# Kernel tuning notes

Measured on AMD Instinct MI355X. Metric: run time of the kernel, lower is better.

The kernel has to match this reference:

```python
import jax, jax.numpy as jnp
import numpy as np

NEIGH_W = 0.25  # self.neigh_w
act = jax.nn.leaky_relu  # negative_slope=0.01, matches nn.LeakyReLU default


def _lin(x, w, b):
    # torch Linear with weight stored as [in, out]
    return x @ w + b


def setup_inputs() -> dict:
    key = jax.random.key(0)
    I, C, L = 1024, 32, 64  # images, curves/image, points/curve (uniform segments)
    N = I * C * L
    ks = jax.random.split(key, 32)

    def p(k, shape, scale=0.1):
        return jax.random.normal(k, shape, dtype=jnp.float32) * scale

    curve_tensor = jax.random.normal(ks[0], (N, 8), dtype=jnp.float32)
    # segment-boundary labels: col1 = curve start (every L rows), col0 = image start (every L*C rows)
    lab = np.zeros((N, 2), np.int64)
    lab[::L, 1] = 1
    lab[::L * C, 0] = 1
    curve_label = jnp.asarray(lab)
    cors_batch = jax.random.normal(ks[1], (I, C, C, 5), dtype=jnp.float32)

    inp = dict(curve_tensor=curve_tensor, curve_label=curve_label, cors_batch=cors_batch)
    dims = [("crv_mlp", 8, 8), ("crv_lv1", 24, 32), ("crv_lv2", 32, 24),
            ("inter1", 24, 24), ("inter2", 24, 24),
            ("grp1", 72, 24), ("grp2", 24, 24), ("grp3", 24, 24),
            ("img1", 24, 18), ("img2", 18, 12), ("img3", 12, 6)]
    for i, (name, din, dout) in enumerate(dims):
        inp[name + "_w"] = p(ks[2 + 2 * i], (din, dout))
        inp[name + "_b"] = p(ks[3 + 2 * i], (dout,))
    # cor_mlp is initialized to all ones (cor_init_rand=0 in the original)
    inp["cor_w"] = jnp.ones((5, 24), jnp.float32)
    inp["cor_b"] = jnp.ones((24,), jnp.float32)
    return inp


def reference(curve_tensor, curve_label, cors_batch,
              crv_mlp_w, crv_mlp_b, crv_lv1_w, crv_lv1_b, crv_lv2_w, crv_lv2_b,
              inter1_w, inter1_b, inter2_w, inter2_b, cor_w, cor_b,
              grp1_w, grp1_b, grp2_w, grp2_b, grp3_w, grp3_b,
              img1_w, img1_b, img2_w, img2_b, img3_w, img3_b):
    I, C = cors_batch.shape[0], cors_batch.shape[1]
    L = curve_tensor.shape[0] // (I * C)

    # ---- curve level: ring-graph roll aggregation within each curve segment ----
    x = curve_tensor.reshape(I * C, L, 8)

    def agg(t):
        neigh = _lin(jnp.roll(t, 1, axis=1), crv_mlp_w, crv_mlp_b) \
              + _lin(jnp.roll(t, -1, axis=1), crv_mlp_w, crv_mlp_b)
        return NEIGH_W * neigh + (1.0 - 2.0 * NEIGH_W) * t

    x1 = agg(x)
    x2 = agg(x1)
    embed = jnp.concatenate([x, x1, x2], axis=-1)            # [I*C, L, 24]
    feat = act(_lin(act(_lin(embed, crv_lv1_w, crv_lv1_b)), crv_lv2_w, crv_lv2_b))
    group = feat.mean(axis=1)                                 # [I*C, 24] per-curve feature
    group = act(_lin(act(_lin(group, inter1_w, inter1_b)), inter2_w, inter2_b))

    # ---- image level: pairwise cor-weighted aggregation over curves per image ----
    g = group.reshape(I, C, 24)
    cor = act(_lin(cors_batch, cor_w, cor_b))                 # [I, C, C, 24]

    def cagg(t):
        # after[i,j,d] = sum_k before[i,k,d] * cor[i,j,k,d]
        return jnp.einsum('ikd,ijkd->ijd', t, cor)

    g1 = cagg(g)
    g2 = cagg(g1)
    emb = jnp.concatenate([g, g1, g2], axis=-1)               # [I, C, 72]
    h = act(_lin(act(_lin(act(_lin(emb, grp1_w, grp1_b)), grp2_w, grp2_b)), grp3_w, grp3_b))
    img = h.mean(axis=1)                                      # [I, 24]

    out = _lin(act(_lin(act(_lin(img, img1_w, img1_b)), img2_w, img2_b)), img3_w, img3_b)
    return jax.nn.sigmoid(out)                                # [I, brands]
```

## Files before the change

### kernel.cpp

```cpp
#include <hip/hip_runtime.h>
#include <hip/hip_bf16.h>
#include <math.h>

#define LEAKY(x) fmaxf((x), 0.01f * (x))

typedef float v2f __attribute__((ext_vector_type(2)));
typedef __bf16 bf8 __attribute__((ext_vector_type(8)));
typedef float f4 __attribute__((ext_vector_type(4)));

constexpr int IMGS = 1024;
constexpr int CRV  = 32;
constexpr int LPT  = 64;

__device__ __forceinline__ void ldseg(float* dst, const float* __restrict__ src,
                                      int n, int tid, int nt) {
  for (int i = tid; i < n; i += nt) dst[i] = src[i];
}

__device__ __forceinline__ f4 leaky4(f4 x) {
  return __builtin_elementwise_max(x, x * 0.01f);
}

__device__ __forceinline__ float ring_sum(float v) {
  int s = __builtin_bit_cast(int, v);
  int a = __builtin_amdgcn_update_dpp(0, s, 0x134, 0xF, 0xF, false);
  int b = __builtin_amdgcn_update_dpp(0, s, 0x13C, 0xF, 0xF, false);
  return __builtin_bit_cast(float, a) + __builtin_bit_cast(float, b);
}

__device__ __forceinline__ float row_sum16(float v) {
  int s;
  s = __builtin_amdgcn_update_dpp(0, __builtin_bit_cast(int, v), 0x121, 0xF, 0xF, false);
  v += __builtin_bit_cast(float, s);
  s = __builtin_amdgcn_update_dpp(0, __builtin_bit_cast(int, v), 0x122, 0xF, 0xF, false);
  v += __builtin_bit_cast(float, s);
  s = __builtin_amdgcn_update_dpp(0, __builtin_bit_cast(int, v), 0x124, 0xF, 0xF, false);
  v += __builtin_bit_cast(float, s);
  s = __builtin_amdgcn_update_dpp(0, __builtin_bit_cast(int, v), 0x128, 0xF, 0xF, false);
  v += __builtin_bit_cast(float, s);
  return v;
}

__device__ __forceinline__ unsigned bfpair(float x, float y) {
  __hip_bfloat162 h = __float22bfloat162_rn(make_float2(x, y));
  unsigned r;
  __builtin_memcpy(&r, &h, 4);
  return r;
}

__device__ __forceinline__ unsigned bfr(float x) {
  unsigned u = __builtin_bit_cast(unsigned, x);
  return u + 0x7fffu + ((u >> 16) & 1u);
}
__device__ __forceinline__ unsigned bfpair_fast(float x, float y) {
  return __builtin_amdgcn_perm(bfr(y), bfr(x), 0x07060302u);
}

#define WOFF(pp, cc) (((pp) << 4) + ((((cc) + ((pp) >> 1)) & 3) << 2))

__device__ float w1eff_val(const float* mw, const float* mb,
                           const float* w1, const float* b1, int n, int k) {
  if (k < 8) {
    return w1[k * 32 + n] + 0.5f * w1[(8 + k) * 32 + n] + 0.25f * w1[(16 + k) * 32 + n];
  } else if (k < 16) {
    int a = k - 8;
    float s = 0.f;
    for (int i = 0; i < 8; i++)
      s += mw[a * 8 + i] * (w1[(8 + i) * 32 + n] + w1[(16 + i) * 32 + n]);
    return 0.25f * s;
  } else if (k < 24) {
    int a = k - 16;
    float s = 0.f;
    for (int i = 0; i < 8; i++) {
      float m2 = 0.f;
      for (int c = 0; c < 8; c++) m2 += mw[a * 8 + c] * mw[c * 8 + i];
      s += m2 * w1[(16 + i) * 32 + n];
    }
    return 0.0625f * s;
  } else if (k == 24) {
    float s = b1[n];
    for (int i = 0; i < 8; i++) {
      s += mb[i] * (0.5f * w1[(8 + i) * 32 + n] + 0.75f * w1[(16 + i) * 32 + n]);
      float wb = 0.f;
      for (int c = 0; c < 8; c++) wb += mb[c] * mw[c * 8 + i];
      s += 0.25f * wb * w1[(16 + i) * 32 + n];
    }
    return s;
  }
  return 0.f;
}

__global__ __launch_bounds__(256) void prep_kernel(
    const float* __restrict__ mw, const float* __restrict__ mb,
    const float* __restrict__ w1, const float* __restrict__ b1,
    const float* __restrict__ w2, const float* __restrict__ b2,
    const float* __restrict__ i1w, const float* __restrict__ i2w,
    unsigned* __restrict__ fragA1, unsigned* __restrict__ fragA2,
    float* __restrict__ fragC,
    float* __restrict__ i1wT, float* __restrict__ i2wT)
{
  const int tid = threadIdx.x;
  for (int idx = tid; idx < 512; idx += 256) {
    int tile = idx >> 8;
    int lane = (idx >> 2) & 63;
    int word = idx & 3;
    int n  = tile * 16 + (lane & 15);
    int k0 = (lane >> 4) * 8 + word * 2;
    fragA1[idx] = bfpair(w1eff_val(mw, mb, w1, b1, n, k0),
                         w1eff_val(mw, mb, w1, b1, n, k0 + 1));
    float u0 = (n < 24) ? w2[k0 * 24 + n] : 0.f;
    float u1 = (n < 24) ? w2[(k0 + 1) * 24 + n] : 0.f;
    fragA2[idx] = bfpair(u0, u1);
  }
  for (int idx = tid; idx < 512; idx += 256) {
    int tile = idx >> 8;
    int lane = (idx >> 2) & 63;
    int r = idx & 3;
    int n = tile * 16 + ((lane >> 4) & 3) * 4 + r;
    fragC[idx] = (n < 24) ? b2[n] : 0.f;
  }
  for (int idx = tid; idx < 576; idx += 256) {
    int jj = idx / 24, ii = idx - jj * 24;
    i1wT[idx] = i1w[ii * 24 + jj];
    i2wT[idx] = i2w[ii * 24 + jj];
  }
}

__global__ __launch_bounds__(256) void curve_kernel(
    const float* __restrict__ ct,
    const unsigned* __restrict__ fragA1, const unsigned* __restrict__ fragA2,
    const float* __restrict__ fragC,
    const float* __restrict__ i1wT, const float* __restrict__ i1b,
    const float* __restrict__ i2wT, const float* __restrict__ i2b,
    float* __restrict__ gout)
{
  __shared__ __align__(16) unsigned sX[4][2][1024];
  __shared__ __align__(16) float    srow[4][2][32];

  const int tid  = threadIdx.x;
  const int wave = tid >> 6;
  const int lane = tid & 63;
  const int curve0 = blockIdx.x * 8 + wave * 2;

  uint4 awv[2], a2v[2];
  float4 cbv[2];
  #pragma unroll
  for (int mt = 0; mt < 2; mt++) {
    awv[mt] = *(const uint4*)(fragA1 + mt * 256 + lane * 4);
    a2v[mt] = *(const uint4*)(fragA2 + mt * 256 + lane * 4);
    cbv[mt] = *(const float4*)(fragC + mt * 256 + lane * 4);
  }

  const float* pA = ct + ((size_t)curve0 * LPT + lane) * 8;
  const float* pB = pA + LPT * 8;
  float4 a0 = *(const float4*)pA;
  float4 a1 = *(const float4*)(pA + 4);
  float4 b0 = *(const float4*)pB;
  float4 b1v = *(const float4*)(pB + 4);

  float xA[8], xB[8];
  xA[0] = a0.x; xA[1] = a0.y; xA[2] = a0.z; xA[3] = a0.w;
  xA[4] = a1.x; xA[5] = a1.y; xA[6] = a1.z; xA[7] = a1.w;
  xB[0] = b0.x; xB[1] = b0.y; xB[2] = b0.z; xB[3] = b0.w;
  xB[4] = b1v.x; xB[5] = b1v.y; xB[6] = b1v.z; xB[7] = b1v.w;

  float s1A[8], t2A[8], s1B[8], t2B[8];
  #pragma unroll
  for (int i = 0; i < 8; i++) s1A[i] = ring_sum(xA[i]);
  #pragma unroll
  for (int i = 0; i < 8; i++) s1B[i] = ring_sum(xB[i]);
  #pragma unroll
  for (int i = 0; i < 8; i++) t2A[i] = ring_sum(s1A[i]);
  #pragma unroll
  for (int i = 0; i < 8; i++) t2B[i] = ring_sum(s1B[i]);

  unsigned* Xw0 = &sX[wave][0][0];
  unsigned* Xw1 = &sX[wave][1][0];
  {
    uint4 wv;
    wv.x = bfpair_fast(xA[0], xA[1]);  wv.y = bfpair_fast(xA[2], xA[3]);
    wv.z = bfpair_fast(xA[4], xA[5]);  wv.w = bfpair_fast(xA[6], xA[7]);
    *(uint4*)&Xw0[WOFF(lane, 0)] = wv;
    wv.x = bfpair_fast(s1A[0], s1A[1]); wv.y = bfpair_fast(s1A[2], s1A[3]);
    wv.z = bfpair_fast(s1A[4], s1A[5]); wv.w = bfpair_fast(s1A[6], s1A[7]);
    *(uint4*)&Xw0[WOFF(lane, 1)] = wv;
    wv.x = bfpair_fast(t2A[0], t2A[1]); wv.y = bfpair_fast(t2A[2], t2A[3]);
    wv.z = bfpair_fast(t2A[4], t2A[5]); wv.w = bfpair_fast(t2A[6], t2A[7]);
    *(uint4*)&Xw0[WOFF(lane, 2)] = wv;
    wv.x = 0x00003f80u; wv.y = 0u; wv.z = 0u; wv.w = 0u;
    *(uint4*)&Xw0[WOFF(lane, 3)] = wv;

    wv.x = bfpair_fast(xB[0], xB[1]);  wv.y = bfpair_fast(xB[2], xB[3]);
    wv.z = bfpair_fast(xB[4], xB[5]);  wv.w = bfpair_fast(xB[6], xB[7]);
    *(uint4*)&Xw1[WOFF(lane, 0)] = wv;
    wv.x = bfpair_fast(s1B[0], s1B[1]); wv.y = bfpair_fast(s1B[2], s1B[3]);
    wv.z = bfpair_fast(s1B[4], s1B[5]); wv.w = bfpair_fast(s1B[6], s1B[7]);
    *(uint4*)&Xw1[WOFF(lane, 1)] = wv;
    wv.x = bfpair_fast(t2B[0], t2B[1]); wv.y = bfpair_fast(t2B[2], t2B[3]);
    wv.z = bfpair_fast(t2B[4], t2B[5]); wv.w = bfpair_fast(t2B[6], t2B[7]);
    *(uint4*)&Xw1[WOFF(lane, 2)] = wv;
    wv.x = 0x00003f80u; wv.y = 0u; wv.z = 0u; wv.w = 0u;
    *(uint4*)&Xw1[WOFF(lane, 3)] = wv;
  }
  __builtin_amdgcn_wave_barrier();

  const int q   = lane >> 4;
  const int c16 = lane & 15;

  #pragma unroll
  for (int cv = 0; cv < 2; cv++) {
    unsigned* Xw = cv ? Xw1 : Xw0;
    f4 d[2][4];
    bf8 bx[4];
    #pragma unroll
    for (int nt = 0; nt < 4; nt++)
      bx[nt] = __builtin_bit_cast(bf8, *(const uint4*)&Xw[WOFF(c16 + nt * 16, q)]);
    const f4 z = (f4){0.f, 0.f, 0.f, 0.f};
    #pragma unroll
    for (int mt = 0; mt < 2; mt++) {
      bf8 aw = __builtin_bit_cast(bf8, awv[mt]);
      #pragma unroll
      for (int nt = 0; nt < 4; nt++)
        d[mt][nt] = __builtin_amdgcn_mfma_f32_16x16x32_bf16(aw, bx[nt], z, 0, 0, 0);
    }
    #pragma unroll
    for (int mt = 0; mt < 2; mt++) {
      #pragma unroll
      for (int nt = 0; nt < 4; nt++) {
        f4 v = leaky4(d[mt][nt]);
        const int prow = nt * 16 + c16;
        const int word = WOFF(prow, mt * 2 + (q >> 1)) + (q & 1) * 2;
        uint2 pk; pk.x = bfpair_fast(v.x, v.y); pk.y = bfpair_fast(v.z, v.w);
        *(uint2*)&Xw[word] = pk;
      }
    }
  }
  __builtin_amdgcn_wave_barrier();

  #pragma unroll
  for (int cv = 0; cv < 2; cv++) {
    unsigned* Xw = cv ? Xw1 : Xw0;
    f4 d2[2][4];
    bf8 bh[4];
    #pragma unroll
    for (int nt = 0; nt < 4; nt++)
      bh[nt] = __builtin_bit_cast(bf8, *(const uint4*)&Xw[WOFF(c16 + nt * 16, q)]);
    #pragma unroll
    for (int mt = 0; mt < 2; mt++) {
      bf8 a2 = __builtin_bit_cast(bf8, a2v[mt]);
      f4 cb_ = __builtin_bit_cast(f4, cbv[mt]);
      #pragma unroll
      for (int nt = 0; nt < 4; nt++)
        d2[mt][nt] = __builtin_amdgcn_mfma_f32_16x16x32_bf16(a2, bh[nt], cb_, 0, 0, 0);
    }
    float m8[2][4];
    #pragma unroll
    for (int mt = 0; mt < 2; mt++) {
      f4 t = leaky4(d2[mt][0]) + leaky4(d2[mt][1]);
      t = t + leaky4(d2[mt][2]);
      t = t + leaky4(d2[mt][3]);
      #pragma unroll
      for (int r = 0; r < 4; r++)
        m8[mt][r] = row_sum16(t[r]) * (1.0f / 64.0f);
    }
    if (c16 == 0) {
      f4 v0 = (f4){m8[0][0], m8[0][1], m8[0][2], m8[0][3]};
      *(f4*)&srow[wave][cv][q * 4] = v0;
      if (q < 2) {
        f4 v1 = (f4){m8[1][0], m8[1][1], m8[1][2], m8[1][3]};
        *(f4*)&srow[wave][cv][16 + q * 4] = v1;
      }
    }
  }
  __builtin_amdgcn_wave_barrier();

  const int half = lane >> 5;
  const int l32  = lane & 31;
  const int jd   = (l32 < 24) ? l32 : 0;
  float* srw = &srow[wave][half][0];

  float sv[24];
  #pragma unroll
  for (int i = 0; i < 24; i++) sv[i] = srw[i];

  float a = i1b[jd];
  #pragma unroll
  for (int t = 0; t < 6; t++) {
    float4 wv = *(const float4*)&i1wT[jd * 24 + t * 4];
    a += sv[t * 4 + 0] * wv.x + sv[t * 4 + 1] * wv.y
       + sv[t * 4 + 2] * wv.z + sv[t * 4 + 3] * wv.w;
  }
  a = LEAKY(a);
  if (l32 < 24) srw[l32] = a;
  __builtin_amdgcn_wave_barrier();

  float av[24];
  #pragma unroll
  for (int i = 0; i < 24; i++) av[i] = srw[i];

  float o = i2b[jd];
  #pragma unroll
  for (int t = 0; t < 6; t++) {
    float4 wv = *(const float4*)&i2wT[jd * 24 + t * 4];
    o += av[t * 4 + 0] * wv.x + av[t * 4 + 1] * wv.y
       + av[t * 4 + 2] * wv.z + av[t * 4 + 3] * wv.w;
  }
  o = LEAKY(o);

  if (l32 < 24) gout[(size_t)(curve0 + half) * 24 + l32] = o;
}

__global__ __launch_bounds__(768) void image_kernel(
    const float* __restrict__ cors, const float* __restrict__ gin,
    const float* __restrict__ cw,  const float* __restrict__ cb,
    const float* __restrict__ g1w, const float* __restrict__ g1b,
    const float* __restrict__ g2w, const float* __restrict__ g2b,
    const float* __restrict__ g3w, const float* __restrict__ g3b,
    const float* __restrict__ m1w, const float* __restrict__ m1b,
    const float* __restrict__ m2w, const float* __restrict__ m2b,
    const float* __restrict__ m3w, const float* __restrict__ m3b,
    float* __restrict__ out)
{
  __shared__ __align__(16) float sCorsP[CRV * CRV * 8];
  __shared__ __align__(16) float sG0[CRV * 24], sG1[CRV * 24], sG2[CRV * 24];
  __shared__ __align__(16) float sHa[CRV * 24], sHb[CRV * 24];
  __shared__ float sW1[1728], sW2[576], sW3[576];
  __shared__ float sT[96];

  const int tid = threadIdx.x;
  const int img = blockIdx.x;
  const int j = tid / 24;
  const int d = tid - j * 24;

  {
    const float* cbase = cors + (size_t)img * (CRV * CRV * 5);
    for (int idx = tid; idx < CRV * CRV * 5; idx += 768) {
      int jj = idx / 160;
      int r  = idx - jj * 160;
      int k  = r / 5;
      int c  = r - k * 5;
      sCorsP[(jj * CRV + k) * 8 + c] = cbase[idx];
    }
  }
  sG0[tid] = gin[(size_t)img * (CRV * 24) + tid];
  ldseg(sW1, g1w, 1728, tid, 768);
  ldseg(sW2, g2w, 576, tid, 768);
  ldseg(sW3, g3w, 576, tid, 768);
  float wc0 = cw[0 * 24 + d], wc1 = cw[1 * 24 + d], wc2 = cw[2 * 24 + d];
  float wc3 = cw[3 * 24 + d], wc4 = cw[4 * 24 + d];
  float cbd = cb[d];
  float g1bd = g1b[d], g2bd = g2b[d], g3bd = g3b[d];
  __syncthreads();

  float corv[CRV];
  #pragma unroll
  for (int k = 0; k < CRV; k++) {
    const float* cr = &sCorsP[(j * CRV + k) * 8];
    float4 qq = *(const float4*)cr;
    float q4 = cr[4];
    float v = cbd + qq.x * wc0 + qq.y * wc1 + qq.z * wc2 + qq.w * wc3 + q4 * wc4;
    corv[k] = LEAKY(v);
  }
  {
    float t1 = 0.0f;
    #pragma unroll
    for (int k = 0; k < CRV; k++) t1 += sG0[k * 24 + d] * corv[k];
    sG1[j * 24 + d] = t1;
  }
  __syncthreads();
  {
    float t2 = 0.0f;
    #pragma unroll
    for (int k = 0; k < CRV; k++) t2 += sG1[k * 24 + d] * corv[k];
    sG2[j * 24 + d] = t2;
  }
  __syncthreads();
  {
    float v = g1bd;
    #pragma unroll
    for (int i = 0; i < 24; i++) v += sG0[j * 24 + i] * sW1[i * 24 + d];
    #pragma unroll
    for (int i = 0; i < 24; i++) v += sG1[j * 24 + i] * sW1[(24 + i) * 24 + d];
    #pragma unroll
    for (int i = 0; i < 24; i++) v += sG2[j * 24 + i] * sW1[(48 + i) * 24 + d];
    sHa[j * 24 + d] = LEAKY(v);
  }
  __syncthreads();
  {
    float v = g2bd;
    #pragma unroll
    for (int i = 0; i < 24; i++) v += sHa[j * 24 + i] * sW2[i * 24 + d];
    sHb[j * 24 + d] = LEAKY(v);
  }
  __syncthreads();
  {
    float v = g3bd;
    #pragma unroll
    for (int i = 0; i < 24; i++) v += sHb[j * 24 + i] * sW3[i * 24 + d];
    sHa[j * 24 + d] = LEAKY(v);
  }
  __syncthreads();
  if (tid < 24) {
    float s = 0.0f;
    #pragma unroll
    for (int k = 0; k < CRV; k++) s += sHa[k * 24 + tid];
    sT[tid] = s * (1.0f / CRV);
  }
  __syncthreads();
  if (tid < 18) {
    float v = m1b[tid];
    #pragma unroll
    for (int i = 0; i < 24; i++) v += sT[i] * m1w[i * 18 + tid];
    sT[32 + tid] = LEAKY(v);
  }
  __syncthreads();
  if (tid < 12) {
    float v = m2b[tid];
    #pragma unroll
    for (int i = 0; i < 18; i++) v += sT[32 + i] * m2w[i * 12 + tid];
    sT[56 + tid] = LEAKY(v);
  }
  __syncthreads();
  if (tid < 6) {
    float v = m3b[tid];
    #pragma unroll
    for (int i = 0; i < 12; i++) v += sT[56 + i] * m3w[i * 6 + tid];
    out[img * 6 + tid] = 1.0f / (1.0f + expf(-v));
  }
}

extern "C" void kernel_launch(void* const* d_in, const int* in_sizes, int n_in,
                              void* d_out, int out_size, void* d_ws, size_t ws_size,
                              hipStream_t stream) {
  const float* ct   = (const float*)d_in[0];
  const float* cors = (const float*)d_in[2];
  const float* mw  = (const float*)d_in[3];
  const float* mb  = (const float*)d_in[4];
  const float* w1  = (const float*)d_in[5];
  const float* b1  = (const float*)d_in[6];
  const float* w2  = (const float*)d_in[7];
  const float* b2  = (const float*)d_in[8];
  const float* i1w = (const float*)d_in[9];
  const float* i1b = (const float*)d_in[10];
  const float* i2w = (const float*)d_in[11];
  const float* i2b = (const float*)d_in[12];

  const float *cw, *cb, *g1w, *g1b, *g2w, *g2b, *g3w, *g3b;
  const float *m1w, *m1b, *m2w, *m2b, *m3w, *m3b;
  if (in_sizes[13] == 120) {
    cw  = (const float*)d_in[13]; cb  = (const float*)d_in[14];
    g1w = (const float*)d_in[15]; g1b = (const float*)d_in[16];
    g2w = (const float*)d_in[17]; g2b = (const float*)d_in[18];
    g3w = (const float*)d_in[19]; g3b = (const float*)d_in[20];
    m1w = (const float*)d_in[21]; m1b = (const float*)d_in[22];
    m2w = (const float*)d_in[23]; m2b = (const float*)d_in[24];
    m3w = (const float*)d_in[25]; m3b = (const float*)d_in[26];
  } else {
    g1w = (const float*)d_in[13]; g1b = (const float*)d_in[14];
    g2w = (const float*)d_in[15]; g2b = (const float*)d_in[16];
    g3w = (const float*)d_in[17]; g3b = (const float*)d_in[18];
    m1w = (const float*)d_in[19]; m1b = (const float*)d_in[20];
    m2w = (const float*)d_in[21]; m2b = (const float*)d_in[22];
    m3w = (const float*)d_in[23]; m3b = (const float*)d_in[24];
    cw  = (const float*)d_in[25]; cb  = (const float*)d_in[26];
  }

  float* wsf = (float*)d_ws;
  float* group = wsf;
  const size_t base = (size_t)IMGS * CRV * 24;
  unsigned* fragA1 = (unsigned*)(wsf + base);
  unsigned* fragA2 = fragA1 + 512;
  float*    fragC  = (float*)(fragA2 + 512);
  float*    i1wT   = fragC + 512;
  float*    i2wT   = i1wT + 576;
  float* out = (float*)d_out;

  prep_kernel<<<1, 256, 0, stream>>>(mw, mb, w1, b1, w2, b2, i1w, i2w,
                                     fragA1, fragA2, fragC, i1wT, i2wT);
  curve_kernel<<<(IMGS * CRV) / 8, 256, 0, stream>>>(
      ct, fragA1, fragA2, fragC, i1wT, i1b, i2wT, i2b, group);
  image_kernel<<<IMGS, 768, 0, stream>>>(
      cors, group, cw, cb, g1w, g1b, g2w, g2b, g3w, g3b,
      m1w, m1b, m2w, m2b, m3w, m3b, out);
}
```

Measured before the change: 220.0 us.

## Fold weight-prep kernel into curve kernel, computing MFMA fragments per block

Removes the single-block prep kernel launch and instead has every curve block compute the folded layer-1 weights, the layer-2 bf16 MFMA fragments and the bias fragment into shared memory, with two block-wide barriers. The intermediate MLP now reads the untransposed weights directly from global memory instead of the transposed copies. This removes one launch and its serialization, at the cost of redundant weight preparation in each of 4096 blocks, added __syncthreads, extra LDS use, and strided scalar weight loads.

```diff
diff --git a/kernel.cpp b/kernel.cpp
--- a/kernel.cpp
+++ b/kernel.cpp
@@ -41,13 +41,6 @@
   return v;
 }
 
-__device__ __forceinline__ unsigned bfpair(float x, float y) {
-  __hip_bfloat162 h = __float22bfloat162_rn(make_float2(x, y));
-  unsigned r;
-  __builtin_memcpy(&r, &h, 4);
-  return r;
-}
-
 __device__ __forceinline__ unsigned bfr(float x) {
   unsigned u = __builtin_bit_cast(unsigned, x);
   return u + 0x7fffu + ((u >> 16) & 1u);
@@ -58,98 +51,24 @@
 
 #define WOFF(pp, cc) (((pp) << 4) + ((((cc) + ((pp) >> 1)) & 3) << 2))
 
-__device__ float w1eff_val(const float* mw, const float* mb,
-                           const float* w1, const float* b1, int n, int k) {
-  if (k < 8) {
-    return w1[k * 32 + n] + 0.5f * w1[(8 + k) * 32 + n] + 0.25f * w1[(16 + k) * 32 + n];
-  } else if (k < 16) {
-    int a = k - 8;
-    float s = 0.f;
-    for (int i = 0; i < 8; i++)
-      s += mw[a * 8 + i] * (w1[(8 + i) * 32 + n] + w1[(16 + i) * 32 + n]);
-    return 0.25f * s;
-  } else if (k < 24) {
-    int a = k - 16;
-    float s = 0.f;
-    for (int i = 0; i < 8; i++) {
-      float m2 = 0.f;
-      for (int c = 0; c < 8; c++) m2 += mw[a * 8 + c] * mw[c * 8 + i];
-      s += m2 * w1[(16 + i) * 32 + n];
-    }
-    return 0.0625f * s;
-  } else if (k == 24) {
-    float s = b1[n];
-    for (int i = 0; i < 8; i++) {
-      s += mb[i] * (0.5f * w1[(8 + i) * 32 + n] + 0.75f * w1[(16 + i) * 32 + n]);
-      float wb = 0.f;
-      for (int c = 0; c < 8; c++) wb += mb[c] * mw[c * 8 + i];
-      s += 0.25f * wb * w1[(16 + i) * 32 + n];
-    }
-    return s;
-  }
-  return 0.f;
-}
-
-__global__ __launch_bounds__(256) void prep_kernel(
-    const float* __restrict__ mw, const float* __restrict__ mb,
-    const float* __restrict__ w1, const float* __restrict__ b1,
-    const float* __restrict__ w2, const float* __restrict__ b2,
-    const float* __restrict__ i1w, const float* __restrict__ i2w,
-    unsigned* __restrict__ fragA1, unsigned* __restrict__ fragA2,
-    float* __restrict__ fragC,
-    float* __restrict__ i1wT, float* __restrict__ i2wT)
-{
-  const int tid = threadIdx.x;
-  for (int idx = tid; idx < 512; idx += 256) {
-    int tile = idx >> 8;
-    int lane = (idx >> 2) & 63;
-    int word = idx & 3;
-    int n  = tile * 16 + (lane & 15);
-    int k0 = (lane >> 4) * 8 + word * 2;
-    fragA1[idx] = bfpair(w1eff_val(mw, mb, w1, b1, n, k0),
-                         w1eff_val(mw, mb, w1, b1, n, k0 + 1));
-    float u0 = (n < 24) ? w2[k0 * 24 + n] : 0.f;
-    float u1 = (n < 24) ? w2[(k0 + 1) * 24 + n] : 0.f;
-    fragA2[idx] = bfpair(u0, u1);
-  }
-  for (int idx = tid; idx < 512; idx += 256) {
-    int tile = idx >> 8;
-    int lane = (idx >> 2) & 63;
-    int r = idx & 3;
-    int n = tile * 16 + ((lane >> 4) & 3) * 4 + r;
-    fragC[idx] = (n < 24) ? b2[n] : 0.f;
-  }
-  for (int idx = tid; idx < 576; idx += 256) {
-    int jj = idx / 24, ii = idx - jj * 24;
-    i1wT[idx] = i1w[ii * 24 + jj];
-    i2wT[idx] = i2w[ii * 24 + jj];
-  }
-}
-
 __global__ __launch_bounds__(256) void curve_kernel(
     const float* __restrict__ ct,
-    const unsigned* __restrict__ fragA1, const unsigned* __restrict__ fragA2,
-    const float* __restrict__ fragC,
-    const float* __restrict__ i1wT, const float* __restrict__ i1b,
-    const float* __restrict__ i2wT, const float* __restrict__ i2b,
+    const float* __restrict__ mw,  const float* __restrict__ mb,
+    const float* __restrict__ w1,  const float* __restrict__ b1,
+    const float* __restrict__ w2,  const float* __restrict__ b2,
+    const float* __restrict__ i1w, const float* __restrict__ i1b,
+    const float* __restrict__ i2w, const float* __restrict__ i2b,
     float* __restrict__ gout)
 {
   __shared__ __align__(16) unsigned sX[4][2][1024];
   __shared__ __align__(16) float    srow[4][2][32];
+  __shared__ __align__(16) unsigned sF1[512], sF2[512];
+  __shared__ float sAux[72];
 
   const int tid  = threadIdx.x;
   const int wave = tid >> 6;
   const int lane = tid & 63;
   const int curve0 = blockIdx.x * 8 + wave * 2;
-
-  uint4 awv[2], a2v[2];
-  float4 cbv[2];
-  #pragma unroll
-  for (int mt = 0; mt < 2; mt++) {
-    awv[mt] = *(const uint4*)(fragA1 + mt * 256 + lane * 4);
-    a2v[mt] = *(const uint4*)(fragA2 + mt * 256 + lane * 4);
-    cbv[mt] = *(const float4*)(fragC + mt * 256 + lane * 4);
-  }
 
   const float* pA = ct + ((size_t)curve0 * LPT + lane) * 8;
   const float* pB = pA + LPT * 8;
@@ -157,6 +76,28 @@
   float4 a1 = *(const float4*)(pA + 4);
   float4 b0 = *(const float4*)pB;
   float4 b1v = *(const float4*)(pB + 4);
+
+  const int q   = lane >> 4;
+  const int c16 = lane & 15;
+
+  float4 cbv[2];
+  cbv[0] = *(const float4*)&b2[q * 4];
+  cbv[1] = (q < 2) ? *(const float4*)&b2[16 + q * 4]
+                   : make_float4(0.f, 0.f, 0.f, 0.f);
+
+  if (tid < 64) {
+    int a = tid >> 3, i = tid & 7;
+    float s = 0.f;
+    #pragma unroll
+    for (int c = 0; c < 8; c++) s += mw[a * 8 + c] * mw[c * 8 + i];
+    sAux[tid] = s;
+  } else if (tid < 72) {
+    int i = tid - 64;
+    float s = 0.f;
+    #pragma unroll
+    for (int c = 0; c < 8; c++) s += mb[c] * mw[c * 8 + i];
+    sAux[tid] = s;
+  }
 
   float xA[8], xB[8];
   xA[0] = a0.x; xA[1] = a0.y; xA[2] = a0.z; xA[3] = a0.w;
@@ -202,10 +143,82 @@
     wv.x = 0x00003f80u; wv.y = 0u; wv.z = 0u; wv.w = 0u;
     *(uint4*)&Xw1[WOFF(lane, 3)] = wv;
   }
-  __builtin_amdgcn_wave_barrier();
-
-  const int q   = lane >> 4;
-  const int c16 = lane & 15;
+  __syncthreads();
+
+  {
+    const int idx   = tid * 2;
+    const int tile  = idx >> 8;
+    const int lane2 = (idx >> 2) & 63;
+    const int word  = idx & 3;
+    const int n     = tile * 16 + (lane2 & 15);
+    const int q2    = lane2 >> 4;
+    const int k0    = q2 * 8 + word * 2;
+
+    float e[4];
+    if (q2 == 0) {
+      #pragma unroll
+      for (int j = 0; j < 4; j++) {
+        int k = k0 + j;
+        e[j] = w1[k * 32 + n] + 0.5f * w1[(8 + k) * 32 + n]
+             + 0.25f * w1[(16 + k) * 32 + n];
+      }
+    } else if (q2 == 1) {
+      float W[8];
+      #pragma unroll
+      for (int i = 0; i < 8; i++)
+        W[i] = w1[(8 + i) * 32 + n] + w1[(16 + i) * 32 + n];
+      #pragma unroll
+      for (int j = 0; j < 4; j++) {
+        int a = k0 - 8 + j;
+        float s = 0.f;
+        #pragma unroll
+        for (int i = 0; i < 8; i++) s += mw[a * 8 + i] * W[i];
+        e[j] = 0.25f * s;
+      }
+    } else if (q2 == 2) {
+      float V[8];
+      #pragma unroll
+      for (int i = 0; i < 8; i++) V[i] = w1[(16 + i) * 32 + n];
+      #pragma unroll
+      for (int j = 0; j < 4; j++) {
+        int a = k0 - 16 + j;
+        float s = 0.f;
+        #pragma unroll
+        for (int i = 0; i < 8; i++) s += sAux[a * 8 + i] * V[i];
+        e[j] = 0.0625f * s;
+      }
+    } else {
+      e[0] = e[1] = e[2] = e[3] = 0.f;
+      if (word == 0) {
+        float s = b1[n];
+        #pragma unroll
+        for (int i = 0; i < 8; i++) {
+          float A = w1[(8 + i) * 32 + n];
+          float B = w1[(16 + i) * 32 + n];
+          s += mb[i] * (0.5f * A + 0.75f * B);
+          s += 0.25f * sAux[64 + i] * B;
+        }
+        e[0] = s;
+      }
+    }
+    sF1[idx]     = bfpair_fast(e[0], e[1]);
+    sF1[idx + 1] = bfpair_fast(e[2], e[3]);
+
+    float u[4];
+    #pragma unroll
+    for (int j = 0; j < 4; j++)
+      u[j] = (n < 24) ? w2[(k0 + j) * 24 + n] : 0.f;
+    sF2[idx]     = bfpair_fast(u[0], u[1]);
+    sF2[idx + 1] = bfpair_fast(u[2], u[3]);
+  }
+  __syncthreads();
+
+  uint4 awv[2], a2v[2];
+  #pragma unroll
+  for (int mt = 0; mt < 2; mt++) {
+    awv[mt] = *(const uint4*)&sF1[mt * 256 + lane * 4];
+    a2v[mt] = *(const uint4*)&sF2[mt * 256 + lane * 4];
+  }
 
   #pragma unroll
   for (int cv = 0; cv < 2; cv++) {
@@ -285,11 +298,7 @@
 
   float a = i1b[jd];
   #pragma unroll
-  for (int t = 0; t < 6; t++) {
-    float4 wv = *(const float4*)&i1wT[jd * 24 + t * 4];
-    a += sv[t * 4 + 0] * wv.x + sv[t * 4 + 1] * wv.y
-       + sv[t * 4 + 2] * wv.z + sv[t * 4 + 3] * wv.w;
-  }
+  for (int i = 0; i < 24; i++) a += sv[i] * i1w[i * 24 + jd];
   a = LEAKY(a);
   if (l32 < 24) srw[l32] = a;
   __builtin_amdgcn_wave_barrier();
@@ -300,11 +309,7 @@
 
   float o = i2b[jd];
   #pragma unroll
-  for (int t = 0; t < 6; t++) {
-    float4 wv = *(const float4*)&i2wT[jd * 24 + t * 4];
-    o += av[t * 4 + 0] * wv.x + av[t * 4 + 1] * wv.y
-       + av[t * 4 + 2] * wv.z + av[t * 4 + 3] * wv.w;
-  }
+  for (int i = 0; i < 24; i++) o += av[i] * i2w[i * 24 + jd];
   o = LEAKY(o);
 
   if (l32 < 24) gout[(size_t)(curve0 + half) * 24 + l32] = o;
@@ -465,20 +470,11 @@
     cw  = (const float*)d_in[25]; cb  = (const float*)d_in[26];
   }
 
-  float* wsf = (float*)d_ws;
-  float* group = wsf;
-  const size_t base = (size_t)IMGS * CRV * 24;
-  unsigned* fragA1 = (unsigned*)(wsf + base);
-  unsigned* fragA2 = fragA1 + 512;
-  float*    fragC  = (float*)(fragA2 + 512);
-  float*    i1wT   = fragC + 512;
-  float*    i2wT   = i1wT + 576;
+  float* group = (float*)d_ws;
   float* out = (float*)d_out;
 
-  prep_kernel<<<1, 256, 0, stream>>>(mw, mb, w1, b1, w2, b2, i1w, i2w,
-                                     fragA1, fragA2, fragC, i1wT, i2wT);
   curve_kernel<<<(IMGS * CRV) / 8, 256, 0, stream>>>(
-      ct, fragA1, fragA2, fragC, i1wT, i1b, i2wT, i2b, group);
+      ct, mw, mb, w1, b1, w2, b2, i1w, i1b, i2w, i2b, group);
   image_kernel<<<IMGS, 768, 0, stream>>>(
       cors, group, cw, cb, g1w, g1b, g2w, g2b, g3w, g3b,
       m1w, m1b, m2w, m2b, m3w, m3b, out);
```

New measurement: 223.0 us. About the same (+1.4%).
